# Optimization experiments

Measured on AMD Instinct MI355X. Metric: run time of the kernel, lower is better.

The kernel has to match this reference:

```python
import jax, jax.numpy as jnp
import numpy as np

B, S, F, T = 32, 512, 512, 1024  # batch, seq_len(channel dim), feat_dim, time length


def setup_inputs() -> dict:
    key = jax.random.key(0)
    ks = jax.random.split(key, 6)
    scale = 0.05  # keep tanh/softmax in a non-saturated regime
    return {
        "z_robot": jax.random.normal(ks[0], (B, S, T), dtype=jnp.float32),
        "z_human": jax.random.normal(ks[1], (B, S, T), dtype=jnp.float32),
        "W_b": jax.random.normal(ks[2], (S, S), dtype=jnp.float32) * scale,
        "W_q": jax.random.normal(ks[3], (F, S), dtype=jnp.float32) * scale,
        "W_v": jax.random.normal(ks[4], (F, S), dtype=jnp.float32) * scale,
        "w_hq": jax.random.normal(ks[5], (1, F), dtype=jnp.float32) * scale,
    }


def reference(z_robot, z_human, W_b, W_q, W_v, w_hq):
    # aux = W_b @ z_human : [B, S, Th]
    aux = jnp.einsum('su,buh->bsh', W_b, z_human)
    # C = tanh(z_robot^T @ aux) : [B, Tr, Th]
    C = jnp.tanh(jnp.einsum('bst,bsh->bth', z_robot, aux))
    # aux2 = W_v @ z_human : [B, F, Th];  aux3 = W_q @ z_robot : [B, F, Tr]
    aux2 = jnp.einsum('fs,bsh->bfh', W_v, z_human)
    aux3 = jnp.einsum('fs,bst->bft', W_q, z_robot)
    # H_q = tanh(aux3 + aux2 @ C^T) : [B, F, Tr]
    H_q = jnp.tanh(aux3 + jnp.einsum('bfh,bth->bft', aux2, C))
    # a_q = softmax(w_hq @ H_q, axis=2) : [B, 1, Tr]
    a_q = jax.nn.softmax(jnp.einsum('of,bft->bot', w_hq, H_q), axis=2)
    # attn = z_robot @ a_q^T : [B, S, 1]
    attn = jnp.einsum('bst,bot->bso', z_robot, a_q)
    return (attn, a_q, C)
```

## Files before the change

### kernel.cpp

```cpp
#include <hip/hip_runtime.h>
#include <math.h>


using f32x4  = __attribute__((ext_vector_type(4))) float;
using bf16x8 = __attribute__((ext_vector_type(8))) short;

__device__ __forceinline__ ushort f2bf(float x) {
    uint u = __float_as_uint(x);
    return (ushort)((u + 0x7fffu + ((u >> 16) & 1u)) >> 16);
}
__device__ __forceinline__ float bf2f(ushort h) { return __uint_as_float((uint)h << 16); }

__device__ __forceinline__ float fast_tanh(float x) {
    return 1.0f - 2.0f / (__expf(2.0f * x) + 1.0f);
}

__device__ __forceinline__ void gll16(const void* g, void* l) {
    __builtin_amdgcn_global_load_lds(
        (__attribute__((address_space(1))) void*)(void*)g,
        (__attribute__((address_space(3))) void*)l, 16, 0, 0);
}

__device__ __forceinline__ void xcd_decode(int id, int tiles_pb, int ntx,
                                           int& batch, int& m0, int& n0) {
    const int xcd = id & 7, slot = id >> 3;
    batch = (slot / tiles_pb) * 8 + xcd;
    const int tile = slot % tiles_pb;
    m0 = (tile / ntx) * 128;
    n0 = (tile % ntx) * 128;
}


__global__ __launch_bounds__(256)
void transpose_split2_k(const float* __restrict__ inA, ushort* __restrict__ hiA,
                        ushort* __restrict__ loA,
                        const float* __restrict__ inB, ushort* __restrict__ hiB,
                        ushort* __restrict__ loB) {
    __shared__ float tile[32][65];
    const int z = blockIdx.z;
    const int b = z & 31, which = z >> 5;
    const float* in = (which ? inB : inA) + (size_t)b * 512 * 1024;
    ushort* hi = (which ? hiB : hiA) + (size_t)b * 512 * 1024;
    ushort* lo = (which ? loB : loA) + (size_t)b * 512 * 1024;
    const int c0 = blockIdx.x * 32, r0 = blockIdx.y * 64;
    const int tx = threadIdx.x, ty = threadIdx.y;
    #pragma unroll
    for (int i = 0; i < 8; ++i)
        tile[tx][ty + 8 * i] = in[(size_t)(r0 + ty + 8 * i) * 1024 + c0 + tx];
    __syncthreads();
    #pragma unroll
    for (int j = 0; j < 4; ++j) {
        const int c = ty + 8 * j;
        const float v0 = tile[c][2 * tx], v1 = tile[c][2 * tx + 1];
        const ushort h0 = f2bf(v0), h1 = f2bf(v1);
        const size_t o = (size_t)(c0 + c) * 512 + r0 + 2 * tx;
        *(ushort2*)&hi[o] = make_ushort2(h0, h1);
        *(ushort2*)&lo[o] = make_ushort2(f2bf(v0 - bf2f(h0)), f2bf(v1 - bf2f(h1)));
    }
}

__global__ __launch_bounds__(256)
void convert_weights_k(const float* __restrict__ Wb, const float* __restrict__ Wq,
                       const float* __restrict__ Wv, ushort* __restrict__ Wb_hi,
                       ushort* __restrict__ Wb_lo, ushort* __restrict__ Wq16,
                       ushort* __restrict__ Wv16) {
    const int i = blockIdx.x * 256 + threadIdx.x;
    const int seg = i >> 18, off = i & 262143;
    if (seg == 0) {
        const float v = Wb[off];
        const ushort h = f2bf(v);
        Wb_hi[off] = h;
        Wb_lo[off] = f2bf(v - bf2f(h));
    } else if (seg == 1) {
        Wq16[off] = f2bf(Wq[off]);
    } else {
        Wv16[off] = f2bf(Wv[off]);
    }
}

template <int MODE>
__global__ __launch_bounds__(256, 2)
void gemm_split(const ushort* __restrict__ Ahi, const ushort* __restrict__ Alo,
                long sAb, int ldA,
                const ushort* __restrict__ Bhi, const ushort* __restrict__ Blo,
                long sBb, int ldB, int K,
                ushort* __restrict__ Ohi, ushort* __restrict__ Olo,
                float* __restrict__ Of, ushort* __restrict__ O16,
                int ldO, long sOb, int tiles_pb, int ntx) {
    __shared__ __align__(16) ushort lds[32768];
    int b, m0, n0;
    xcd_decode(blockIdx.x, tiles_pb, ntx, b, m0, n0);
    const int t = threadIdx.x, l = t & 63, w = t >> 6, wm = w >> 1, wn = w & 1;

    const int srow = l >> 2;
    const int sch  = ((l & 3) ^ (srow & 3)) * 8;
    const ushort* pAh = Ahi + (long)b * sAb + (long)(m0 + w * 32 + srow) * ldA + sch;
    const ushort* pAl = Alo + (long)b * sAb + (long)(m0 + w * 32 + srow) * ldA + sch;
    const ushort* pBh = Bhi + (long)b * sBb + (long)(n0 + w * 32 + srow) * ldB + sch;
    const ushort* pBl = Blo + (long)b * sBb + (long)(n0 + w * 32 + srow) * ldB + sch;

    const int q = l >> 4;
    int offA[4], offB[4];
    #pragma unroll
    for (int i = 0; i < 4; ++i) {
        const int rA = wm * 64 + i * 16 + (l & 15);
        offA[i] = rA * 32 + (q ^ (rA & 3)) * 8;
        const int rB = wn * 64 + i * 16 + (l & 15);
        offB[i] = rB * 32 + (q ^ (rB & 3)) * 8;
    }

    auto stage = [&](int k0, int st) {
        const int base = st * 16384;
        #pragma unroll
        for (int tt = 0; tt < 2; ++tt) {
            const int lo_ = base + (w * 32 + tt * 16) * 32;
            gll16(pAh + (long)(tt * 16) * ldA + k0, lds + lo_);
            gll16(pAl + (long)(tt * 16) * ldA + k0, lds + 4096 + lo_);
            gll16(pBh + (long)(tt * 16) * ldB + k0, lds + 8192 + lo_);
            gll16(pBl + (long)(tt * 16) * ldB + k0, lds + 12288 + lo_);
        }
    };

    f32x4 acc[4][4] = {};
    stage(0, 0);
    int st = 0;
    for (int k0 = 0; k0 < K; k0 += 32) {
        __syncthreads();
        if (k0 + 32 < K) stage(k0 + 32, st ^ 1);
        const int base = st * 16384;
        bf16x8 ah[4], al4[4], bh[4], bl4[4];
        #pragma unroll
        for (int i = 0; i < 4; ++i) {
            ah[i]  = *(const bf16x8*)&lds[base + offA[i]];
            al4[i] = *(const bf16x8*)&lds[base + 4096 + offA[i]];
            bh[i]  = *(const bf16x8*)&lds[base + 8192 + offB[i]];
            bl4[i] = *(const bf16x8*)&lds[base + 12288 + offB[i]];
        }
        #pragma unroll
        for (int i = 0; i < 4; ++i)
            #pragma unroll
            for (int j = 0; j < 4; ++j) {
                acc[i][j] = __builtin_amdgcn_mfma_f32_16x16x32_bf16(ah[i],  bh[j],  acc[i][j], 0, 0, 0);
                acc[i][j] = __builtin_amdgcn_mfma_f32_16x16x32_bf16(ah[i],  bl4[j], acc[i][j], 0, 0, 0);
                acc[i][j] = __builtin_amdgcn_mfma_f32_16x16x32_bf16(al4[i], bh[j],  acc[i][j], 0, 0, 0);
            }
        st ^= 1;
    }

    const int cl = l & 15, rl = (l >> 4) * 4;
    #pragma unroll
    for (int i = 0; i < 4; ++i)
        #pragma unroll
        for (int r = 0; r < 4; ++r) {
            const long mg = m0 + wm * 64 + i * 16 + rl + r;
            #pragma unroll
            for (int j = 0; j < 4; ++j) {
                const int ng = n0 + wn * 64 + j * 16 + cl;
                const float v = acc[i][j][r];
                const long o = (long)b * sOb + mg * ldO + ng;
                if (MODE == 0) {
                    const ushort h = f2bf(v);
                    Ohi[o] = h;
                    Olo[o] = f2bf(v - bf2f(h));
                } else {
                    const float tv = fast_tanh(v);
                    Of[o] = tv;
                    O16[o] = f2bf(tv);
                }
            }
        }
}

__device__ __forceinline__ void plain_core(
    const ushort* __restrict__ A, long sAb, int ldA,
    const ushort* __restrict__ B, long sBb, int ldB, int K,
    int b, int m0, int n0, ushort* lds, f32x4 (&acc)[4][4]) {
    const int t = threadIdx.x, l = t & 63, w = t >> 6, wm = w >> 1, wn = w & 1;
    const int srow = l >> 3;
    const int sch  = ((l & 7) ^ (srow & 7)) * 8;
    const ushort* pA = A + (long)b * sAb + (long)(m0 + w * 32 + srow) * ldA + sch;
    const ushort* pB = B + (long)b * sBb + (long)(n0 + w * 32 + srow) * ldB + sch;
    const int q = l >> 4;
    int offA[4], offB[4];
    #pragma unroll
    for (int i = 0; i < 4; ++i) {
        const int rA = wm * 64 + i * 16 + (l & 15);
        offA[i] = rA * 64 + (q ^ (rA & 7)) * 8;
        const int rB = wn * 64 + i * 16 + (l & 15);
        offB[i] = 8192 + rB * 64 + (q ^ (rB & 7)) * 8;
    }
    auto stage = [&](int k0, int st) {
        const int base = st * 16384;
        #pragma unroll
        for (int tt = 0; tt < 4; ++tt) {
            gll16(pA + (long)(tt * 8) * ldA + k0, lds + base + (w * 32 + tt * 8) * 64);
            gll16(pB + (long)(tt * 8) * ldB + k0, lds + base + 8192 + (w * 32 + tt * 8) * 64);
        }
    };
    stage(0, 0);
    int st = 0;
    for (int k0 = 0; k0 < K; k0 += 64) {
        __syncthreads();
        if (k0 + 64 < K) stage(k0 + 64, st ^ 1);
        const int base = st * 16384;
        #pragma unroll
        for (int s = 0; s < 2; ++s) {
            bf16x8 av[4], bv[4];
            #pragma unroll
            for (int i = 0; i < 4; ++i) {
                av[i] = *(const bf16x8*)&lds[base + (offA[i] ^ (s * 32))];
                bv[i] = *(const bf16x8*)&lds[base + (offB[i] ^ (s * 32))];
            }
            #pragma unroll
            for (int i = 0; i < 4; ++i)
                #pragma unroll
                for (int j = 0; j < 4; ++j)
                    acc[i][j] = __builtin_amdgcn_mfma_f32_16x16x32_bf16(av[i], bv[j], acc[i][j], 0, 0, 0);
        }
        st ^= 1;
    }
    __syncthreads();
}

__global__ __launch_bounds__(256, 2)
void gemm_plain_store(const ushort* __restrict__ A, long sAb, int ldA,
                      const ushort* __restrict__ B, long sBb, int ldB, int K,
                      ushort* __restrict__ O, long sOb, int ldO,
                      int tiles_pb, int ntx) {
    __shared__ __align__(16) ushort lds[32768];
    int b, m0, n0;
    xcd_decode(blockIdx.x, tiles_pb, ntx, b, m0, n0);
    f32x4 acc[4][4] = {};
    plain_core(A, sAb, ldA, B, sBb, ldB, K, b, m0, n0, lds, acc);
    const int t = threadIdx.x, l = t & 63, w = t >> 6, wm = w >> 1, wn = w & 1;
    const int cl = l & 15, rl = (l >> 4) * 4;
    #pragma unroll
    for (int i = 0; i < 4; ++i)
        #pragma unroll
        for (int r = 0; r < 4; ++r) {
            const long mg = m0 + wm * 64 + i * 16 + rl + r;
            #pragma unroll
            for (int j = 0; j < 4; ++j)
                O[(long)b * sOb + mg * ldO + n0 + wn * 64 + j * 16 + cl] = f2bf(acc[i][j][r]);
        }
}

__global__ __launch_bounds__(256, 2)
void gemm_fused_logits(const ushort* __restrict__ Wq16, const ushort* __restrict__ zrT,
                       const ushort* __restrict__ aux2, const ushort* __restrict__ C16,
                       const float* __restrict__ whq, float* __restrict__ logits,
                       int tiles_pb, int ntx) {
    __shared__ __align__(16) ushort lds[32768];
    int b, m0, n0;
    xcd_decode(blockIdx.x, tiles_pb, ntx, b, m0, n0);
    f32x4 acc[4][4] = {};
    plain_core(Wq16, 0, 512, zrT, 524288, 512, 512, b, m0, n0, lds, acc);
    plain_core(aux2, 524288, 1024, C16, 1048576, 1024, 1024, b, m0, n0, lds, acc);
    const int t = threadIdx.x, l = t & 63, w = t >> 6, wm = w >> 1, wn = w & 1;
    float p[4] = {0.f, 0.f, 0.f, 0.f};
    #pragma unroll
    for (int i = 0; i < 4; ++i)
        #pragma unroll
        for (int r = 0; r < 4; ++r) {
            const float wv = whq[m0 + wm * 64 + i * 16 + (l >> 4) * 4 + r];
            #pragma unroll
            for (int j = 0; j < 4; ++j)
                p[j] += wv * fast_tanh(acc[i][j][r]);
        }
    #pragma unroll
    for (int j = 0; j < 4; ++j) {
        p[j] += __shfl_xor(p[j], 16);
        p[j] += __shfl_xor(p[j], 32);
    }
    float* red = (float*)lds;
    if (l < 16) {
        #pragma unroll
        for (int j = 0; j < 4; ++j)
            red[wm * 128 + wn * 64 + j * 16 + l] = p[j];
    }
    __syncthreads();
    if (t < 128)
        atomicAdd(&logits[(long)b * 1024 + n0 + t], red[t] + red[128 + t]);
}

__global__ __launch_bounds__(256)
void softmax_kernel(const float* __restrict__ logits, float* __restrict__ aq, int T) {
    __shared__ float sm[256];
    const int b = blockIdx.x, tid = threadIdx.x;
    float v[4];
    float mx = -1e30f;
    #pragma unroll
    for (int i = 0; i < 4; ++i) {
        v[i] = logits[(size_t)b * T + tid + 256 * i];
        mx = fmaxf(mx, v[i]);
    }
    sm[tid] = mx; __syncthreads();
    for (int s = 128; s > 0; s >>= 1) {
        if (tid < s) sm[tid] = fmaxf(sm[tid], sm[tid + s]);
        __syncthreads();
    }
    mx = sm[0]; __syncthreads();
    float e[4], sum = 0.f;
    #pragma unroll
    for (int i = 0; i < 4; ++i) { e[i] = __expf(v[i] - mx); sum += e[i]; }
    sm[tid] = sum; __syncthreads();
    for (int s = 128; s > 0; s >>= 1) {
        if (tid < s) sm[tid] += sm[tid + s];
        __syncthreads();
    }
    const float inv = 1.0f / sm[0];
    #pragma unroll
    for (int i = 0; i < 4; ++i)
        aq[(size_t)b * T + tid + 256 * i] = e[i] * inv;
}

__global__ __launch_bounds__(256)
void attn_kernel(const float* __restrict__ ZR, const float* __restrict__ aq,
                 float* __restrict__ out, int S, int T) {
    const int b = blockIdx.y;
    const int s = blockIdx.x * 4 + (threadIdx.x >> 6);
    const int lane = threadIdx.x & 63;
    const float* row = ZR + ((size_t)b * S + s) * T;
    const float* a = aq + (size_t)b * T;
    float sum = 0.f;
    for (int t = lane; t < T; t += 64) sum += row[t] * a[t];
    #pragma unroll
    for (int off = 32; off > 0; off >>= 1) sum += __shfl_down(sum, off, 64);
    if (lane == 0) out[(size_t)b * S + s] = sum;
}

#define BM 64
#define BN 64
#define BK 16
#define PAD 4

__global__ __launch_bounds__(256)
void gemm_nn(const float* __restrict__ A, const float* __restrict__ Bm,
             float* __restrict__ D, int M, int N, int K) {
    __shared__ float As[BK][BM + PAD];
    __shared__ float Bs[BK][BN + PAD];
    const int b = blockIdx.z, m0 = blockIdx.y * BM, n0 = blockIdx.x * BN;
    const int tx = threadIdx.x, ty = threadIdx.y, f = ty * 16 + tx;
    const float* Bb = Bm + (size_t)b * K * N;
    float acc[4][4] = {};
    const int ka = f % 16, ma = f / 16, nb = f % 64, kb = f / 64;
    for (int k0 = 0; k0 < K; k0 += BK) {
        #pragma unroll
        for (int i = 0; i < 4; ++i)
            As[ka][ma + 16 * i] = A[(size_t)(m0 + ma + 16 * i) * K + k0 + ka];
        #pragma unroll
        for (int i = 0; i < 4; ++i)
            Bs[kb + 4 * i][nb] = Bb[(size_t)(k0 + kb + 4 * i) * N + n0 + nb];
        __syncthreads();
        #pragma unroll
        for (int k = 0; k < BK; ++k) {
            float av[4], bv[4];
            *(float4*)av = *(const float4*)&As[k][ty * 4];
            *(float4*)bv = *(const float4*)&Bs[k][tx * 4];
            #pragma unroll
            for (int i = 0; i < 4; ++i)
                #pragma unroll
                for (int j = 0; j < 4; ++j) acc[i][j] += av[i] * bv[j];
        }
        __syncthreads();
    }
    float* Db = D + (size_t)b * M * N;
    #pragma unroll
    for (int i = 0; i < 4; ++i)
        *(float4*)&Db[(size_t)(m0 + ty * 4 + i) * N + n0 + tx * 4] =
            make_float4(acc[i][0], acc[i][1], acc[i][2], acc[i][3]);
}

__global__ __launch_bounds__(256)
void gemm_tn_tanh(const float* __restrict__ ZR, const float* __restrict__ AUX,
                  float* __restrict__ C, int M, int N, int K) {
    __shared__ float As[BK][BM + PAD];
    __shared__ float Bs[BK][BN + PAD];
    const int b = blockIdx.z, m0 = blockIdx.y * BM, n0 = blockIdx.x * BN;
    const int tx = threadIdx.x, ty = threadIdx.y, f = ty * 16 + tx;
    const float* ZRb = ZR + (size_t)b * K * M;
    const float* AUXb = AUX + (size_t)b * K * N;
    float acc[4][4] = {};
    const int nl = f % 64, kl = f / 64;
    for (int k0 = 0; k0 < K; k0 += BK) {
        #pragma unroll
        for (int i = 0; i < 4; ++i)
            As[kl + 4 * i][nl] = ZRb[(size_t)(k0 + kl + 4 * i) * M + m0 + nl];
        #pragma unroll
        for (int i = 0; i < 4; ++i)
            Bs[kl + 4 * i][nl] = AUXb[(size_t)(k0 + kl + 4 * i) * N + n0 + nl];
        __syncthreads();
        #pragma unroll
        for (int k = 0; k < BK; ++k) {
            float av[4], bv[4];
            *(float4*)av = *(const float4*)&As[k][ty * 4];
            *(float4*)bv = *(const float4*)&Bs[k][tx * 4];
            #pragma unroll
            for (int i = 0; i < 4; ++i)
                #pragma unroll
                for (int j = 0; j < 4; ++j) acc[i][j] += av[i] * bv[j];
        }
        __syncthreads();
    }
    float* Cb = C + (size_t)b * M * N;
    #pragma unroll
    for (int i = 0; i < 4; ++i)
        *(float4*)&Cb[(size_t)(m0 + ty * 4 + i) * N + n0 + tx * 4] =
            make_float4(fast_tanh(acc[i][0]), fast_tanh(acc[i][1]),
                        fast_tanh(acc[i][2]), fast_tanh(acc[i][3]));
}

__global__ __launch_bounds__(256)
void gemm_nt_fused(const float* __restrict__ Wq, const float* __restrict__ ZR,
                   const float* __restrict__ A2, const float* __restrict__ Cm,
                   const float* __restrict__ whq, float* __restrict__ logits,
                   int M, int N, int K1, int K2) {
    __shared__ float As[BK][BM + PAD];
    __shared__ float Bs[BK][BN + PAD];
    __shared__ float red[16][BN];
    const int b = blockIdx.z, m0 = blockIdx.y * BM, n0 = blockIdx.x * BN;
    const int tx = threadIdx.x, ty = threadIdx.y, f = ty * 16 + tx;
    const float* ZRb = ZR + (size_t)b * K1 * N;
    const float* A2b = A2 + (size_t)b * M * K2;
    const float* Cb = Cm + (size_t)b * N * K2;
    float acc3[4][4] = {};
    {
        const int ka = f % 16, ma = f / 16, nb = f % 64, kb = f / 64;
        for (int k0 = 0; k0 < K1; k0 += BK) {
            #pragma unroll
            for (int i = 0; i < 4; ++i)
                As[ka][ma + 16 * i] = Wq[(size_t)(m0 + ma + 16 * i) * K1 + k0 + ka];
            #pragma unroll
            for (int i = 0; i < 4; ++i)
                Bs[kb + 4 * i][nb] = ZRb[(size_t)(k0 + kb + 4 * i) * N + n0 + nb];
            __syncthreads();
            #pragma unroll
            for (int k = 0; k < BK; ++k) {
                float av[4], bv[4];
                *(float4*)av = *(const float4*)&As[k][ty * 4];
                *(float4*)bv = *(const float4*)&Bs[k][tx * 4];
                #pragma unroll
                for (int i = 0; i < 4; ++i)
                    #pragma unroll
                    for (int j = 0; j < 4; ++j) acc3[i][j] += av[i] * bv[j];
            }
            __syncthreads();
        }
    }
    float acc[4][4] = {};
    {
        const int ka = f % 16, ra = f / 16;
        for (int k0 = 0; k0 < K2; k0 += BK) {
            #pragma unroll
            for (int i = 0; i < 4; ++i)
                As[ka][ra + 16 * i] = A2b[(size_t)(m0 + ra + 16 * i) * K2 + k0 + ka];
            #pragma unroll
            for (int i = 0; i < 4; ++i)
                Bs[ka][ra + 16 * i] = Cb[(size_t)(n0 + ra + 16 * i) * K2 + k0 + ka];
            __syncthreads();
            #pragma unroll
            for (int k = 0; k < BK; ++k) {
                float av[4], bv[4];
                *(float4*)av = *(const float4*)&As[k][ty * 4];
                *(float4*)bv = *(const float4*)&Bs[k][tx * 4];
                #pragma unroll
                for (int i = 0; i < 4; ++i)
                    #pragma unroll
                    for (int j = 0; j < 4; ++j) acc[i][j] += av[i] * bv[j];
            }
            __syncthreads();
        }
    }
    float p[4] = {0.f, 0.f, 0.f, 0.f};
    #pragma unroll
    for (int i = 0; i < 4; ++i) {
        const float wv = whq[m0 + ty * 4 + i];
        #pragma unroll
        for (int j = 0; j < 4; ++j) p[j] += wv * fast_tanh(acc3[i][j] + acc[i][j]);
    }
    #pragma unroll
    for (int j = 0; j < 4; ++j) red[ty][tx * 4 + j] = p[j];
    __syncthreads();
    if (f < BN) {
        float s = 0.f;
        #pragma unroll
        for (int r = 0; r < 16; ++r) s += red[r][f];
        atomicAdd(&logits[(size_t)b * N + n0 + f], s);
    }
}

extern "C" void kernel_launch(void* const* d_in, const int* in_sizes, int n_in,
                              void* d_out, int out_size, void* d_ws, size_t ws_size,
                              hipStream_t stream) {
    const float* z_robot = (const float*)d_in[0];
    const float* z_human = (const float*)d_in[1];
    const float* W_b     = (const float*)d_in[2];
    const float* W_q     = (const float*)d_in[3];
    const float* W_v     = (const float*)d_in[4];
    const float* w_hq    = (const float*)d_in[5];
    float* out = (float*)d_out;

    const int Bn = 32, S = 512, T = 1024;
    float* attn_out = out;
    float* aq_out   = out + (size_t)Bn * S;
    float* C_out    = out + (size_t)Bn * S + (size_t)Bn * T;

    char* ws = (char*)d_ws;
    const size_t E2 = 33554432;

    ushort* zhT_hi  = (ushort*)(ws);
    ushort* zhT_lo  = (ushort*)(ws + E2);
    ushort* zrT_hi  = (ushort*)(ws + 2 * E2);
    ushort* zrT_lo  = (ushort*)(ws + 3 * E2);
    ushort* auxT_hi = (ushort*)(ws + 4 * E2);
    ushort* auxT_lo = (ushort*)(ws + 5 * E2);
    ushort* C16     = (ushort*)(ws + 6 * E2);
    ushort* aux2    = auxT_hi;
    ushort* Wb_hi   = (ushort*)(ws + 8 * E2);
    ushort* Wb_lo   = Wb_hi + 262144;
    ushort* Wq16    = Wb_hi + 524288;
    ushort* Wv16    = Wb_hi + 786432;
    float*  logitsF = (float*)(ws + 8 * E2 + 2097152);
    const size_t FAST_REQ = 8 * E2 + 2097152 + 131072;

    if (ws_size >= FAST_REQ) {
        hipMemsetAsync(logitsF, 0, (size_t)Bn * T * sizeof(float), stream);
        transpose_split2_k<<<dim3(32, 8, 64), dim3(32, 8), 0, stream>>>(
            z_human, zhT_hi, zhT_lo, z_robot, zrT_hi, zrT_lo);
        convert_weights_k<<<dim3(3072), dim3(256), 0, stream>>>(
            W_b, W_q, W_v, Wb_hi, Wb_lo, Wq16, Wv16);
        gemm_split<0><<<dim3(32 * 32), dim3(256), 0, stream>>>(
            zhT_hi, zhT_lo, 524288, 512, Wb_hi, Wb_lo, 0, 512, 512,
            auxT_hi, auxT_lo, nullptr, nullptr, 512, 524288, 32, 4);
        gemm_split<1><<<dim3(32 * 64), dim3(256), 0, stream>>>(
            zrT_hi, zrT_lo, 524288, 512, auxT_hi, auxT_lo, 524288, 512, 512,
            nullptr, nullptr, C_out, C16, 1024, 1048576, 64, 8);
        gemm_plain_store<<<dim3(32 * 32), dim3(256), 0, stream>>>(
            Wv16, 0, 512, zhT_hi, 524288, 512, 512, aux2, 524288, 1024, 32, 8);
        gemm_fused_logits<<<dim3(32 * 32), dim3(256), 0, stream>>>(
            Wq16, zrT_hi, aux2, C16, w_hq, logitsF, 32, 8);
        softmax_kernel<<<dim3(Bn), dim3(256), 0, stream>>>(logitsF, aq_out, T);
        attn_kernel<<<dim3(S / 4, Bn), dim3(256), 0, stream>>>(z_robot, aq_out, attn_out, S, T);
    } else {
        float* ws0    = (float*)ws;
        float* logits = (float*)(ws + (size_t)Bn * S * T * 4);
        hipMemsetAsync(logits, 0, (size_t)Bn * T * sizeof(float), stream);
        dim3 blk(16, 16);
        gemm_nn<<<dim3(T / BN, S / BM, Bn), blk, 0, stream>>>(W_b, z_human, ws0, S, T, S);
        gemm_tn_tanh<<<dim3(T / BN, T / BM, Bn), blk, 0, stream>>>(z_robot, ws0, C_out, T, T, S);
        gemm_nn<<<dim3(T / BN, 512 / BM, Bn), blk, 0, stream>>>(W_v, z_human, ws0, 512, T, S);
        gemm_nt_fused<<<dim3(T / BN, 512 / BM, Bn), blk, 0, stream>>>(
            W_q, z_robot, ws0, C_out, w_hq, logits, 512, T, S, T);
        softmax_kernel<<<dim3(Bn), dim3(256), 0, stream>>>(logits, aq_out, T);
        attn_kernel<<<dim3(S / 4, Bn), dim3(256), 0, stream>>>(z_robot, aq_out, attn_out, S, T);
    }
}
```

Baseline: 558.3 us.

## Drop LDS double buffering in GEMMs to raise occupancy and fix swizzle

Replaces the double-buffered LDS staging in the split and plain GEMM cores with a single buffer, synchronised by two barriers per k-step. This halves shared memory per block to 32 KB and removes the min-blocks launch bound, so more blocks can be resident per CU. It also changes the XOR swizzle in the split GEMM to use bits 1-2 of the row, aiming to cut LDS bank conflicts. The cost is that global loads no longer overlap with MFMA work inside a block, so latency hiding now relies on other resident blocks.

```diff
diff --git a/kernel.cpp b/kernel.cpp
--- a/kernel.cpp
+++ b/kernel.cpp
@@ -79,7 +79,7 @@
 }
 
 template <int MODE>
-__global__ __launch_bounds__(256, 2)
+__global__ __launch_bounds__(256)
 void gemm_split(const ushort* __restrict__ Ahi, const ushort* __restrict__ Alo,
                 long sAb, int ldA,
                 const ushort* __restrict__ Bhi, const ushort* __restrict__ Blo,
@@ -87,13 +87,13 @@
                 ushort* __restrict__ Ohi, ushort* __restrict__ Olo,
                 float* __restrict__ Of, ushort* __restrict__ O16,
                 int ldO, long sOb, int tiles_pb, int ntx) {
-    __shared__ __align__(16) ushort lds[32768];
+    __shared__ __align__(16) ushort lds[16384];
     int b, m0, n0;
     xcd_decode(blockIdx.x, tiles_pb, ntx, b, m0, n0);
     const int t = threadIdx.x, l = t & 63, w = t >> 6, wm = w >> 1, wn = w & 1;
 
     const int srow = l >> 2;
-    const int sch  = ((l & 3) ^ (srow & 3)) * 8;
+    const int sch  = ((l & 3) ^ ((l >> 3) & 3)) * 8;
     const ushort* pAh = Ahi + (long)b * sAb + (long)(m0 + w * 32 + srow) * ldA + sch;
     const ushort* pAl = Alo + (long)b * sAb + (long)(m0 + w * 32 + srow) * ldA + sch;
     const ushort* pBh = Bhi + (long)b * sBb + (long)(n0 + w * 32 + srow) * ldB + sch;
@@ -104,37 +104,29 @@
     #pragma unroll
     for (int i = 0; i < 4; ++i) {
         const int rA = wm * 64 + i * 16 + (l & 15);
-        offA[i] = rA * 32 + (q ^ (rA & 3)) * 8;
+        offA[i] = rA * 32 + (q ^ ((rA >> 1) & 3)) * 8;
         const int rB = wn * 64 + i * 16 + (l & 15);
-        offB[i] = rB * 32 + (q ^ (rB & 3)) * 8;
-    }
-
-    auto stage = [&](int k0, int st) {
-        const int base = st * 16384;
+        offB[i] = rB * 32 + (q ^ ((rB >> 1) & 3)) * 8;
+    }
+
+    f32x4 acc[4][4] = {};
+    for (int k0 = 0; k0 < K; k0 += 32) {
         #pragma unroll
         for (int tt = 0; tt < 2; ++tt) {
-            const int lo_ = base + (w * 32 + tt * 16) * 32;
+            const int lo_ = (w * 32 + tt * 16) * 32;
             gll16(pAh + (long)(tt * 16) * ldA + k0, lds + lo_);
             gll16(pAl + (long)(tt * 16) * ldA + k0, lds + 4096 + lo_);
             gll16(pBh + (long)(tt * 16) * ldB + k0, lds + 8192 + lo_);
             gll16(pBl + (long)(tt * 16) * ldB + k0, lds + 12288 + lo_);
         }
-    };
-
-    f32x4 acc[4][4] = {};
-    stage(0, 0);
-    int st = 0;
-    for (int k0 = 0; k0 < K; k0 += 32) {
-        __syncthreads();
-        if (k0 + 32 < K) stage(k0 + 32, st ^ 1);
-        const int base = st * 16384;
+        __syncthreads();
         bf16x8 ah[4], al4[4], bh[4], bl4[4];
         #pragma unroll
         for (int i = 0; i < 4; ++i) {
-            ah[i]  = *(const bf16x8*)&lds[base + offA[i]];
-            al4[i] = *(const bf16x8*)&lds[base + 4096 + offA[i]];
-            bh[i]  = *(const bf16x8*)&lds[base + 8192 + offB[i]];
-            bl4[i] = *(const bf16x8*)&lds[base + 12288 + offB[i]];
+            ah[i]  = *(const bf16x8*)&lds[offA[i]];
+            al4[i] = *(const bf16x8*)&lds[4096 + offA[i]];
+            bh[i]  = *(const bf16x8*)&lds[8192 + offB[i]];
+            bl4[i] = *(const bf16x8*)&lds[12288 + offB[i]];
         }
         #pragma unroll
         for (int i = 0; i < 4; ++i)
@@ -144,7 +136,7 @@
                 acc[i][j] = __builtin_amdgcn_mfma_f32_16x16x32_bf16(ah[i],  bl4[j], acc[i][j], 0, 0, 0);
                 acc[i][j] = __builtin_amdgcn_mfma_f32_16x16x32_bf16(al4[i], bh[j],  acc[i][j], 0, 0, 0);
             }
-        st ^= 1;
+        __syncthreads();
     }
 
     const int cl = l & 15, rl = (l >> 4) * 4;
@@ -189,27 +181,20 @@
         const int rB = wn * 64 + i * 16 + (l & 15);
         offB[i] = 8192 + rB * 64 + (q ^ (rB & 7)) * 8;
     }
-    auto stage = [&](int k0, int st) {
-        const int base = st * 16384;
+    for (int k0 = 0; k0 < K; k0 += 64) {
         #pragma unroll
         for (int tt = 0; tt < 4; ++tt) {
-            gll16(pA + (long)(tt * 8) * ldA + k0, lds + base + (w * 32 + tt * 8) * 64);
-            gll16(pB + (long)(tt * 8) * ldB + k0, lds + base + 8192 + (w * 32 + tt * 8) * 64);
-        }
-    };
-    stage(0, 0);
-    int st = 0;
-    for (int k0 = 0; k0 < K; k0 += 64) {
-        __syncthreads();
-        if (k0 + 64 < K) stage(k0 + 64, st ^ 1);
-        const int base = st * 16384;
+            gll16(pA + (long)(tt * 8) * ldA + k0, lds + (w * 32 + tt * 8) * 64);
+            gll16(pB + (long)(tt * 8) * ldB + k0, lds + 8192 + (w * 32 + tt * 8) * 64);
+        }
+        __syncthreads();
         #pragma unroll
         for (int s = 0; s < 2; ++s) {
             bf16x8 av[4], bv[4];
             #pragma unroll
             for (int i = 0; i < 4; ++i) {
-                av[i] = *(const bf16x8*)&lds[base + (offA[i] ^ (s * 32))];
-                bv[i] = *(const bf16x8*)&lds[base + (offB[i] ^ (s * 32))];
+                av[i] = *(const bf16x8*)&lds[offA[i] ^ (s * 32)];
+                bv[i] = *(const bf16x8*)&lds[offB[i] ^ (s * 32)];
             }
             #pragma unroll
             for (int i = 0; i < 4; ++i)
@@ -217,17 +202,16 @@
                 for (int j = 0; j < 4; ++j)
                     acc[i][j] = __builtin_amdgcn_mfma_f32_16x16x32_bf16(av[i], bv[j], acc[i][j], 0, 0, 0);
         }
-        st ^= 1;
-    }
-    __syncthreads();
-}
-
-__global__ __launch_bounds__(256, 2)
+        __syncthreads();
+    }
+}
+
+__global__ __launch_bounds__(256)
 void gemm_plain_store(const ushort* __restrict__ A, long sAb, int ldA,
                       const ushort* __restrict__ B, long sBb, int ldB, int K,
                       ushort* __restrict__ O, long sOb, int ldO,
                       int tiles_pb, int ntx) {
-    __shared__ __align__(16) ushort lds[32768];
+    __shared__ __align__(16) ushort lds[16384];
     int b, m0, n0;
     xcd_decode(blockIdx.x, tiles_pb, ntx, b, m0, n0);
     f32x4 acc[4][4] = {};
@@ -245,12 +229,12 @@
         }
 }
 
-__global__ __launch_bounds__(256, 2)
+__global__ __launch_bounds__(256)
 void gemm_fused_logits(const ushort* __restrict__ Wq16, const ushort* __restrict__ zrT,
                        const ushort* __restrict__ aux2, const ushort* __restrict__ C16,
                        const float* __restrict__ whq, float* __restrict__ logits,
                        int tiles_pb, int ntx) {
-    __shared__ __align__(16) ushort lds[32768];
+    __shared__ __align__(16) ushort lds[16384];
     int b, m0, n0;
     xcd_decode(blockIdx.x, tiles_pb, ntx, b, m0, n0);
     f32x4 acc[4][4] = {};
```

After: 591.5 us. +6.0%, slower.
